# Optimization experiments

Hardware: AMD Instinct MI355X
Metric: run time of the kernel (lower is better)

## Reference

```python
import jax, jax.numpy as jnp
import numpy as np

NUM_EMBEDDINGS = 512
EMBEDDING_DIM = 64
COMMITMENT_COST = 0.25
N_TOKENS = 262144


def setup_inputs() -> dict:
    key = jax.random.key(0)
    kz, kc = jax.random.split(key)
    z = jax.random.normal(kz, (N_TOKENS, EMBEDDING_DIM), dtype=jnp.float32)
    # nn.Embedding weight init: uniform(-1/num_embeddings, 1/num_embeddings)
    codebook = jax.random.uniform(
        kc, (NUM_EMBEDDINGS, EMBEDDING_DIM), dtype=jnp.float32,
        minval=-1.0 / NUM_EMBEDDINGS, maxval=1.0 / NUM_EMBEDDINGS)
    return {"z": z, "codebook": codebook}


def reference(z, codebook):
    # squared L2 distances: [N, K]
    distances = (jnp.sum(z * z, axis=1, keepdims=True)
                 + jnp.sum(codebook * codebook, axis=1)
                 - 2.0 * z @ codebook.T)
    encoding_indices = jnp.argmin(distances, axis=1)  # [N]
    z_q = codebook[encoding_indices]                  # [N, D] gather

    e_latent_loss = jnp.mean((jax.lax.stop_gradient(z_q) - z) ** 2)
    q_latent_loss = jnp.mean((z_q - jax.lax.stop_gradient(z)) ** 2)
    loss = q_latent_loss + COMMITMENT_COST * e_latent_loss

    # straight-through estimator
    z_q_st = z + jax.lax.stop_gradient(z_q - z)
    return (z_q_st, loss)
```

## Files before the change

### kernel.cpp

```cpp
#include <hip/hip_runtime.h>
#include <hip/hip_bf16.h>

#define N_TOKENS   262144
#define DIM        64
#define KCODES     512
#define OUT_ELEMS  (N_TOKENS * DIM)
#define LOSS_SCALE (1.25f / 16777216.0f)

typedef float  f32x4 __attribute__((ext_vector_type(4)));
typedef float  f32x8 __attribute__((ext_vector_type(8)));
typedef short  s16x8 __attribute__((ext_vector_type(8)));
typedef unsigned short u16x8 __attribute__((ext_vector_type(8)));

static __device__ __forceinline__ unsigned short f2bf(float f) {
    unsigned int u = __builtin_bit_cast(unsigned int, f);
    u += 0x7fffu + ((u >> 16) & 1u);
    return (unsigned short)(u >> 16);
}

__global__ void vq_prep(const float* __restrict__ cb,
                        unsigned short* __restrict__ cbf,
                        float* __restrict__ c2,
                        float* __restrict__ out_loss) {
    const int k = blockIdx.x;
    const int d = threadIdx.x;
    const float v = cb[k * DIM + d];
    float s = v * v;
    #pragma unroll
    for (int sh = 1; sh < 64; sh <<= 1) s += __shfl_xor(s, sh, 64);
    if (d == 0) c2[k] = s + 2.0f;

    const int t = k >> 4, li = k & 15;
    const int kk = d >> 5, hi = (d >> 3) & 3, j = d & 7;
    const int slot = (t * 2 + kk) * 64 + hi * 16 + li;
    cbf[slot * 8 + j] = f2bf(-2.0f * v);

    if (k == 0 && d == 0) *out_loss = 0.0f;
}

__global__ __launch_bounds__(1024, 4) void vq_main(
    const float* __restrict__ z,
    const float* __restrict__ cb,
    const unsigned short* __restrict__ cbf,
    const float* __restrict__ c2g,
    float* __restrict__ out)
{
    __shared__ unsigned short cbs[KCODES * DIM];
    __shared__ float c2s[KCODES];
    __shared__ int   keysl[16][32];
    __shared__ float lpart[16];

    const int tid  = threadIdx.x;
    const int wave = tid >> 6;
    const int lane = tid & 63;
    const int li   = lane & 15;
    const int hi   = lane >> 4;

    #pragma unroll
    for (int i = 0; i < 4; ++i)
        ((u16x8*)cbs)[i * 1024 + tid] = ((const u16x8*)cbf)[i * 1024 + tid];
    if (tid < KCODES) c2s[tid] = c2g[tid];
    __syncthreads();

    const int token0 = blockIdx.x * 512 + wave * 32;
    float lossp = 0.f;

    s16x8 af[2][2];
    float z2[2];
    #pragma unroll
    for (int m = 0; m < 2; ++m) {
        float zs = 0.f;
        #pragma unroll
        for (int kk = 0; kk < 2; ++kk) {
            const float* p = z + (size_t)(token0 + m * 16 + li) * DIM + kk * 32 + hi * 8;
            const f32x8 v = *(const f32x8*)p;
            s16x8 a;
            #pragma unroll
            for (int j = 0; j < 8; ++j) {
                zs += v[j] * v[j];
                a[j] = (short)f2bf(v[j]);
            }
            af[m][kk] = a;
        }
        zs += __shfl_xor(zs, 16, 64);
        zs += __shfl_xor(zs, 32, 64);
        z2[m] = zs;
    }

    unsigned bkey[2][4];
    #pragma unroll
    for (int m = 0; m < 2; ++m)
        #pragma unroll
        for (int r = 0; r < 4; ++r) bkey[m][r] = 0xFFFFFFFFu;

    #pragma unroll 4
    for (int t = 0; t < 32; ++t) {
        const s16x8 b0 = *(const s16x8*)&cbs[((t * 2 + 0) * 64 + lane) * 8];
        const s16x8 b1 = *(const s16x8*)&cbs[((t * 2 + 1) * 64 + lane) * 8];
        const float cv = c2s[t * 16 + li];
        const unsigned code = (unsigned)(t * 16 + li);
        #pragma unroll
        for (int m = 0; m < 2; ++m) {
            f32x4 acc = {cv, cv, cv, cv};
            acc = __builtin_amdgcn_mfma_f32_16x16x32_bf16(af[m][0], b0, acc, 0, 0, 0);
            acc = __builtin_amdgcn_mfma_f32_16x16x32_bf16(af[m][1], b1, acc, 0, 0, 0);
            #pragma unroll
            for (int r = 0; r < 4; ++r) {
                const unsigned key = (__builtin_bit_cast(unsigned, acc[r]) & ~511u) | code;
                if (key < bkey[m][r]) bkey[m][r] = key;
            }
        }
    }

    #pragma unroll
    for (int sh = 1; sh < 16; sh <<= 1) {
        #pragma unroll
        for (int m = 0; m < 2; ++m)
            #pragma unroll
            for (int r = 0; r < 4; ++r) {
                const unsigned ok = (unsigned)__shfl_xor((int)bkey[m][r], sh, 64);
                if (ok < bkey[m][r]) bkey[m][r] = ok;
            }
    }

    if (li == 0) {
        #pragma unroll
        for (int m = 0; m < 2; ++m)
            #pragma unroll
            for (int r = 0; r < 4; ++r)
                keysl[wave][m * 16 + hi * 4 + r] = (int)bkey[m][r];
    }

    #pragma unroll
    for (int m = 0; m < 2; ++m) {
        const unsigned key = (unsigned)keysl[wave][m * 16 + li];
        const int code = (int)(key & 511u);
        if (hi == 0)
            lossp += (__builtin_bit_cast(float, key & ~511u) - 2.0f) + z2[m];
        const float* cbr = cb + code * DIM + hi * 8;
        const f32x8 q0 = *(const f32x8*)(cbr);
        const f32x8 q1 = *(const f32x8*)(cbr + 32);
        float* op = out + (size_t)(token0 + m * 16 + li) * DIM + hi * 8;
        *(f32x8*)(op)      = q0;
        *(f32x8*)(op + 32) = q1;
    }

    #pragma unroll
    for (int sh = 1; sh < 64; sh <<= 1) lossp += __shfl_xor(lossp, sh, 64);
    if (lane == 0) lpart[wave] = lossp;
    __syncthreads();
    if (tid == 0) {
        float s = 0.f;
        #pragma unroll
        for (int w = 0; w < 16; ++w) s += lpart[w];
        atomicAdd(out + OUT_ELEMS, s * LOSS_SCALE);
    }
}

extern "C" void kernel_launch(void* const* d_in, const int* in_sizes, int n_in,
                              void* d_out, int out_size, void* d_ws, size_t ws_size,
                              hipStream_t stream) {
    const float* z  = (const float*)d_in[0];
    const float* cb = (const float*)d_in[1];
    float* out = (float*)d_out;

    unsigned short* cbf = (unsigned short*)d_ws;
    float* c2 = (float*)((char*)d_ws + KCODES * DIM * sizeof(unsigned short));

    vq_prep<<<KCODES, 64, 0, stream>>>(cb, cbf, c2, out + OUT_ELEMS);
    vq_main<<<N_TOKENS / 512, 1024, 0, stream>>>(z, cb, cbf, c2, out);
}
```

Before: 39.96 us.

## Switch distance MFMA to FP8 with scaled codebook and smaller blocks

Replaces the bf16 MFMA distance computation with FP8 (16x16x32 fp8_fp8). The codebook and norms are prescaled by 256 and 128 so the tiny codebook values stay representable, and the loss is rescaled afterwards. Blocks shrink from 1024 to 512 threads, and the z loads are issued before the codebook copy to LDS so they overlap. FP8 halves the LDS footprint and operand bandwidth, but the much lower precision risks wrong argmin choices on near-ties, and every block still reloads the full codebook.

After: 37.80 us. 1.06x faster.

```diff
diff --git a/kernel.cpp b/kernel.cpp
--- a/kernel.cpp
+++ b/kernel.cpp
@@ -9,17 +9,20 @@
 
 typedef float  f32x4 __attribute__((ext_vector_type(4)));
 typedef float  f32x8 __attribute__((ext_vector_type(8)));
-typedef short  s16x8 __attribute__((ext_vector_type(8)));
-typedef unsigned short u16x8 __attribute__((ext_vector_type(8)));
+typedef int    i32x4 __attribute__((ext_vector_type(4)));
+typedef int    i32x2 __attribute__((ext_vector_type(2)));
 
-static __device__ __forceinline__ unsigned short f2bf(float f) {
-    unsigned int u = __builtin_bit_cast(unsigned int, f);
-    u += 0x7fffu + ((u >> 16) & 1u);
-    return (unsigned short)(u >> 16);
+static __device__ __forceinline__ long pack_fp8x8(const f32x8 v) {
+    int lo = __builtin_amdgcn_cvt_pk_fp8_f32(v[0], v[1], 0, false);
+    lo     = __builtin_amdgcn_cvt_pk_fp8_f32(v[2], v[3], lo, true);
+    int hi = __builtin_amdgcn_cvt_pk_fp8_f32(v[4], v[5], 0, false);
+    hi     = __builtin_amdgcn_cvt_pk_fp8_f32(v[6], v[7], hi, true);
+    i32x2 r = {lo, hi};
+    return __builtin_bit_cast(long, r);
 }
 
 __global__ void vq_prep(const float* __restrict__ cb,
-                        unsigned short* __restrict__ cbf,
+                        unsigned char* __restrict__ cbf,
                         float* __restrict__ c2,
                         float* __restrict__ out_loss) {
     const int k = blockIdx.x;
@@ -28,27 +31,28 @@
     float s = v * v;
     #pragma unroll
     for (int sh = 1; sh < 64; sh <<= 1) s += __shfl_xor(s, sh, 64);
-    if (d == 0) c2[k] = s + 2.0f;
+    if (d == 0) c2[k] = 128.0f * s + 256.0f;
 
     const int t = k >> 4, li = k & 15;
     const int kk = d >> 5, hi = (d >> 3) & 3, j = d & 7;
     const int slot = (t * 2 + kk) * 64 + hi * 16 + li;
-    cbf[slot * 8 + j] = f2bf(-2.0f * v);
+    const int p = __builtin_amdgcn_cvt_pk_fp8_f32(-256.0f * v, 0.0f, 0, false);
+    cbf[slot * 8 + j] = (unsigned char)(p & 0xFF);
 
     if (k == 0 && d == 0) *out_loss = 0.0f;
 }
 
-__global__ __launch_bounds__(1024, 4) void vq_main(
+__global__ __launch_bounds__(512, 4) void vq_main(
     const float* __restrict__ z,
     const float* __restrict__ cb,
-    const unsigned short* __restrict__ cbf,
+    const unsigned char* __restrict__ cbf,
     const float* __restrict__ c2g,
     float* __restrict__ out)
 {
-    __shared__ unsigned short cbs[KCODES * DIM];
+    __shared__ unsigned char cbs[KCODES * DIM];
     __shared__ float c2s[KCODES];
-    __shared__ int   keysl[16][32];
-    __shared__ float lpart[16];
+    __shared__ int   keysl[8][32];
+    __shared__ float lpart[8];
 
     const int tid  = threadIdx.x;
     const int wave = tid >> 6;
@@ -56,36 +60,42 @@
     const int li   = lane & 15;
     const int hi   = lane >> 4;
 
+    const int token0 = blockIdx.x * 256 + wave * 32;
+
+    const float* zb = z + (size_t)token0 * DIM + li * DIM + hi * 8;
+    const f32x8 v00 = *(const f32x8*)(zb);
+    const f32x8 v01 = *(const f32x8*)(zb + 32);
+    const f32x8 v10 = *(const f32x8*)(zb + 16 * DIM);
+    const f32x8 v11 = *(const f32x8*)(zb + 16 * DIM + 32);
+
     #pragma unroll
     for (int i = 0; i < 4; ++i)
-        ((u16x8*)cbs)[i * 1024 + tid] = ((const u16x8*)cbf)[i * 1024 + tid];
-    if (tid < KCODES) c2s[tid] = c2g[tid];
-    __syncthreads();
+        ((i32x4*)cbs)[i * 512 + tid] = ((const i32x4*)cbf)[i * 512 + tid];
+    c2s[tid] = c2g[tid];
 
-    const int token0 = blockIdx.x * 512 + wave * 32;
-    float lossp = 0.f;
-
-    s16x8 af[2][2];
+    long af[2][2];
     float z2[2];
-    #pragma unroll
-    for (int m = 0; m < 2; ++m) {
+    {
         float zs = 0.f;
         #pragma unroll
-        for (int kk = 0; kk < 2; ++kk) {
-            const float* p = z + (size_t)(token0 + m * 16 + li) * DIM + kk * 32 + hi * 8;
-            const f32x8 v = *(const f32x8*)p;
-            s16x8 a;
-            #pragma unroll
-            for (int j = 0; j < 8; ++j) {
-                zs += v[j] * v[j];
-                a[j] = (short)f2bf(v[j]);
-            }
-            af[m][kk] = a;
-        }
+        for (int j = 0; j < 8; ++j) zs += v00[j] * v00[j] + v01[j] * v01[j];
+        af[0][0] = pack_fp8x8(v00);
+        af[0][1] = pack_fp8x8(v01);
         zs += __shfl_xor(zs, 16, 64);
         zs += __shfl_xor(zs, 32, 64);
-        z2[m] = zs;
+        z2[0] = zs;
     }
+    {
+        float zs = 0.f;
+        #pragma unroll
+        for (int j = 0; j < 8; ++j) zs += v10[j] * v10[j] + v11[j] * v11[j];
+        af[1][0] = pack_fp8x8(v10);
+        af[1][1] = pack_fp8x8(v11);
+        zs += __shfl_xor(zs, 16, 64);
+        zs += __shfl_xor(zs, 32, 64);
+        z2[1] = zs;
+    }
+    __syncthreads();
 
     unsigned bkey[2][4];
     #pragma unroll
@@ -95,15 +105,15 @@
 
     #pragma unroll 4
     for (int t = 0; t < 32; ++t) {
-        const s16x8 b0 = *(const s16x8*)&cbs[((t * 2 + 0) * 64 + lane) * 8];
-        const s16x8 b1 = *(const s16x8*)&cbs[((t * 2 + 1) * 64 + lane) * 8];
+        const long b0 = *(const long*)&cbs[((t * 2 + 0) * 64 + lane) * 8];
+        const long b1 = *(const long*)&cbs[((t * 2 + 1) * 64 + lane) * 8];
         const float cv = c2s[t * 16 + li];
         const unsigned code = (unsigned)(t * 16 + li);
         #pragma unroll
         for (int m = 0; m < 2; ++m) {
             f32x4 acc = {cv, cv, cv, cv};
-            acc = __builtin_amdgcn_mfma_f32_16x16x32_bf16(af[m][0], b0, acc, 0, 0, 0);
-            acc = __builtin_amdgcn_mfma_f32_16x16x32_bf16(af[m][1], b1, acc, 0, 0, 0);
+            acc = __builtin_amdgcn_mfma_f32_16x16x32_fp8_fp8(af[m][0], b0, acc, 0, 0, 0);
+            acc = __builtin_amdgcn_mfma_f32_16x16x32_fp8_fp8(af[m][1], b1, acc, 0, 0, 0);
             #pragma unroll
             for (int r = 0; r < 4; ++r) {
                 const unsigned key = (__builtin_bit_cast(unsigned, acc[r]) & ~511u) | code;
@@ -131,12 +141,15 @@
                 keysl[wave][m * 16 + hi * 4 + r] = (int)bkey[m][r];
     }
 
+    float lossp = 0.f;
     #pragma unroll
     for (int m = 0; m < 2; ++m) {
         const unsigned key = (unsigned)keysl[wave][m * 16 + li];
         const int code = (int)(key & 511u);
-        if (hi == 0)
-            lossp += (__builtin_bit_cast(float, key & ~511u) - 2.0f) + z2[m];
+        if (hi == 0) {
+            const float kf = __builtin_bit_cast(float, key & ~511u);
+            lossp += __builtin_fmaf(kf - 256.0f, 0.0078125f, z2[m]);
+        }
         const float* cbr = cb + code * DIM + hi * 8;
         const f32x8 q0 = *(const f32x8*)(cbr);
         const f32x8 q1 = *(const f32x8*)(cbr + 32);
@@ -152,7 +165,7 @@
     if (tid == 0) {
         float s = 0.f;
         #pragma unroll
-        for (int w = 0; w < 16; ++w) s += lpart[w];
+        for (int w = 0; w < 8; ++w) s += lpart[w];
         atomicAdd(out + OUT_ELEMS, s * LOSS_SCALE);
     }
 }
@@ -164,9 +177,9 @@
     const float* cb = (const float*)d_in[1];
     float* out = (float*)d_out;
 
-    unsigned short* cbf = (unsigned short*)d_ws;
-    float* c2 = (float*)((char*)d_ws + KCODES * DIM * sizeof(unsigned short));
+    unsigned char* cbf = (unsigned char*)d_ws;
+    float* c2 = (float*)((char*)d_ws + KCODES * DIM);
 
     vq_prep<<<KCODES, 64, 0, stream>>>(cb, cbf, c2, out + OUT_ELEMS);
-    vq_main<<<N_TOKENS / 512, 1024, 0, stream>>>(z, cb, cbf, c2, out);
+    vq_main<<<N_TOKENS / 256, 512, 0, stream>>>(z, cb, cbf, c2, out);
 }
```
